# Kernel tuning notes

Hardware: AMD Instinct MI355X
Metric: run time of the kernel (lower is better)

The kernel has to match this reference:

```python
import jax, jax.numpy as jnp
import numpy as np

N, E, R, D_IN, D_H, D_OUT = 75000, 1200000, 8, 64, 64, 40


def setup_inputs() -> dict:
    key = jax.random.key(0)
    k_x, k_idx, k_rel, k_w1, k_w2 = jax.random.split(key, 5)
    x = jax.random.normal(k_x, (N, D_IN), dtype=jnp.float32)
    # Regular-degree CSR pointer: ptr[i+1]-ptr[i] = E//N = 16 (nondecreasing, ptr[0]=0, ptr[N]=E)
    ptr = jnp.arange(N + 1, dtype=jnp.int32) * (E // N)
    idx = jax.random.randint(k_idx, (E,), 0, N, dtype=jnp.int32)   # source node per edge
    rel = jax.random.randint(k_rel, (E,), 0, R, dtype=jnp.int32)   # relation type per edge
    W1 = jax.random.normal(k_w1, (R, D_IN, D_H), dtype=jnp.float32) / np.float32(np.sqrt(D_IN))
    W2 = jax.random.normal(k_w2, (R, D_H, D_OUT), dtype=jnp.float32) / np.float32(np.sqrt(D_H))
    return {"x": x, "ptr": ptr, "idx": idx, "rel": rel, "W1": W1, "W2": W2}


def _rgcn_conv(x, W, idx, rel, dst, num_node):
    # Typed transform for every (node, relation) pair: [N, R, F_out]
    xw = jnp.einsum('nd,rdf->nrf', x, W)
    # Per-edge gather of the relation-specific transformed source feature: [E, F_out]
    msg = xw[idx, rel]
    # Scatter-add into destination nodes (CSR rows)
    return jax.ops.segment_sum(msg, dst, num_segments=num_node)


def reference(x, ptr, idx, rel, W1, W2):
    num_edges = idx.shape[0]
    num_node = ptr.shape[0] - 1
    # CSR row id for each edge e: dst[e] = i s.t. ptr[i] <= e < ptr[i+1]
    dst = jnp.searchsorted(ptr, jnp.arange(num_edges, dtype=ptr.dtype), side='right') - 1
    h = _rgcn_conv(x, W1, idx, rel, dst, num_node)
    h = jax.nn.relu(h)  # dropout is identity in eval mode
    h = _rgcn_conv(h, W2, idx, rel, dst, num_node)
    return jax.nn.log_softmax(h, axis=-1)
```

## Files before the change

### kernel.cpp

```cpp
#include <hip/hip_runtime.h>
#include <hip/hip_bf16.h>


typedef __attribute__((ext_vector_type(8))) short short8;
typedef __attribute__((ext_vector_type(4))) float floatx4;

static __device__ __forceinline__ unsigned short f2bf(float f) {
    unsigned u = __float_as_uint(f);
    u += 0x7FFFu + ((u >> 16) & 1u);
    return (unsigned short)(u >> 16);
}
static __device__ __forceinline__ float bflo(unsigned u) { return __uint_as_float(u << 16); }
static __device__ __forceinline__ float bfhi(unsigned u) { return __uint_as_float(u & 0xffff0000u); }

static __device__ __forceinline__ int sgm(int d) {
    return ((d & 12) << 2) | ((d & 48) >> 2) | (d & 3);
}

__global__ void k_packw(const float* __restrict__ W1, const float* __restrict__ W2,
                        unsigned short* __restrict__ BTf1, unsigned short* __restrict__ BTf2) {
    int i = blockIdx.x * 256 + threadIdx.x;
    if (i < 32768) {
        int chunk = i >> 9, w = i & 511;
        int cb = chunk >> 3, k0 = (chunk >> 2) & 1, g = chunk & 3;
        int lg = w >> 7, lr = (w >> 3) & 15, s = w & 7;
        int j = cb * 64 + g * 16 + lr;
        int d = k0 * 32 + lg * 8 + s;
        int r = j >> 6, f = j & 63;
        BTf1[i] = f2bf(W1[r * 4096 + d * 64 + f]);
    } else if (i < 32768 + 20480) {
        int ii = i - 32768;
        int chunk = ii >> 9, w = ii & 511;
        int cb = chunk >> 3, k0 = (chunk >> 2) & 1, g = chunk & 3;
        int lg = w >> 7, lr = (w >> 3) & 15, s = w & 7;
        int j = cb * 64 + g * 16 + lr;
        int d = k0 * 32 + lg * 8 + s;
        int r = j / 40, f = j - r * 40;
        BTf2[ii] = f2bf(W2[r * 2560 + sgm(d) * 40 + f]);
    }
}

template <int AF32, int NSLAB>
__global__ __launch_bounds__(256) void k_xw(
    const void* __restrict__ Av, const unsigned short* __restrict__ BTf,
    unsigned short* __restrict__ xw, int M) {
    constexpr int NC = NSLAB * 64;
    __shared__ short Bs[NSLAB * 4096];

#pragma unroll
    for (int off = 0; off < NSLAB * 4096; off += 2048)
        *(short8*)(Bs + off + threadIdx.x * 8) =
            *(const short8*)((const short*)BTf + off + threadIdx.x * 8);

    int wave = threadIdx.x >> 6, lane = threadIdx.x & 63;
    int lr = lane & 15, lg = lane >> 4;
    int rowbase = (blockIdx.x * 4 + wave) * 16;
    int row = rowbase + lr;

    short8 af[2];
#pragma unroll
    for (int k0 = 0; k0 < 2; ++k0) {
        int koff = k0 * 32 + lg * 8;
        if constexpr (AF32) {
            const float* Af = (const float*)Av;
            float4 v0 = {0, 0, 0, 0}, v1 = {0, 0, 0, 0};
            if (row < M) {
                v0 = *(const float4*)(Af + (size_t)row * 64 + koff);
                v1 = *(const float4*)(Af + (size_t)row * 64 + koff + 4);
            }
            short8 t;
            t[0] = (short)f2bf(v0.x); t[1] = (short)f2bf(v0.y);
            t[2] = (short)f2bf(v0.z); t[3] = (short)f2bf(v0.w);
            t[4] = (short)f2bf(v1.x); t[5] = (short)f2bf(v1.y);
            t[6] = (short)f2bf(v1.z); t[7] = (short)f2bf(v1.w);
            af[k0] = t;
        } else {
            const unsigned short* Ab = (const unsigned short*)Av;
            af[k0] = *(const short8*)(Ab + (size_t)row * 64 + koff);
        }
    }

    __syncthreads();

#pragma unroll
    for (int cb = 0; cb < NSLAB; ++cb) {
        int col0 = cb * 64;
        floatx4 acc[4] = {};
#pragma unroll
        for (int k0 = 0; k0 < 2; ++k0) {
#pragma unroll
            for (int g = 0; g < 4; ++g) {
                short8 b = *(const short8*)(Bs + ((cb * 2 + k0) * 4 + g) * 512 + lane * 8);
                acc[g] = __builtin_amdgcn_mfma_f32_16x16x32_bf16(b, af[k0], acc[g], 0, 0, 0);
            }
        }
        if constexpr (AF32) {
            short8 o0, o1;
#pragma unroll
            for (int g = 0; g < 2; ++g)
#pragma unroll
                for (int i = 0; i < 4; ++i) {
                    o0[g * 4 + i] = (short)f2bf(acc[g][i]);
                    o1[g * 4 + i] = (short)f2bf(acc[g + 2][i]);
                }
            unsigned short* p = xw + (size_t)row * NC + col0 + lg * 16;
            *(short8*)p = o0;
            *(short8*)(p + 8) = o1;
        } else {
#pragma unroll
            for (int g = 0; g < 4; ++g) {
                unsigned lo = ((unsigned)f2bf(acc[g][1]) << 16) | f2bf(acc[g][0]);
                unsigned hi = ((unsigned)f2bf(acc[g][3]) << 16) | f2bf(acc[g][2]);
                uint2 o = {lo, hi};
                *(uint2*)(xw + (size_t)row * NC + col0 + g * 16 + lg * 4) = o;
            }
        }
    }
}

__global__ __launch_bounds__(256) void k_gs_relu(
    const unsigned short* __restrict__ xw,
    const int* __restrict__ ptr, const int* __restrict__ idx,
    const int* __restrict__ rel,
    unsigned short* __restrict__ H, int M, int MP) {
    int rowA = (blockIdx.x * 4 + (threadIdx.x >> 6)) * 2;
    if (rowA >= MP) return;
    rowA = __builtin_amdgcn_readfirstlane(rowA);
    int lane = threadIdx.x & 63;
    int fl = lane & 31, eo = lane >> 5;
    int rowB = rowA + 1;
    int myrow = eo ? rowB : rowA;
    if (rowA >= M) {
        *(unsigned*)(H + (size_t)myrow * 64 + fl * 2) = 0;
        return;
    }
    float cx = 0.f, cy = 0.f;
    bool both = (rowB < M);
    int p0 = ptr[rowA], p1 = ptr[rowA + 1];
    int p2 = both ? ptr[rowA + 2] : p1;
    if (both && (p1 - p0 == 16) && (p2 - p1 == 16)) {
        const int* ia = idx + p0; const int* ra_ = rel + p0;
        const int* ib = idx + p1; const int* rb_ = rel + p1;
        unsigned u[16];
#pragma unroll
        for (int t = 0; t < 16; ++t) {
            unsigned bA = ((unsigned)ia[t] * 8u + (unsigned)ra_[t]) * 128u;
            unsigned bB = ((unsigned)ib[t] * 8u + (unsigned)rb_[t]) * 128u;
            unsigned b = eo ? bB : bA;
            u[t] = *(const unsigned*)((const char*)xw + b + fl * 4);
        }
#pragma unroll
        for (int t = 0; t < 16; ++t) { cx += bflo(u[t]); cy += bfhi(u[t]); }
    } else {
        int ps = 0, deg = 0;
        if (myrow < M) { ps = ptr[myrow]; deg = ptr[myrow + 1] - ps; }
        for (int t = 0; t < deg; ++t) {
            unsigned b = ((unsigned)idx[ps + t] * 8u + (unsigned)rel[ps + t]) * 128u;
            unsigned u = *(const unsigned*)((const char*)xw + b + fl * 4);
            cx += bflo(u); cy += bfhi(u);
        }
    }
    unsigned o = ((unsigned)f2bf(fmaxf(cy, 0.f)) << 16) | f2bf(fmaxf(cx, 0.f));
    *(unsigned*)(H + (size_t)myrow * 64 + fl * 2) = o;
}

__global__ __launch_bounds__(256) void k_gs_lsm(
    const unsigned short* __restrict__ xw,
    const int* __restrict__ ptr, const int* __restrict__ idx,
    const int* __restrict__ rel,
    float* __restrict__ out, int M) {
    int rowA = (blockIdx.x * 4 + (threadIdx.x >> 6)) * 2;
    if (rowA >= M) return;
    rowA = __builtin_amdgcn_readfirstlane(rowA);
    int lane = threadIdx.x & 63;
    int fl = lane & 31, eo = lane >> 5;
    int rowB = rowA + 1;
    int myrow = eo ? rowB : rowA;
    bool okf = fl < 20;
    int flc = okf ? fl : 0;
    float cx = 0.f, cy = 0.f;
    bool both = (rowB < M);
    int p0 = ptr[rowA], p1 = ptr[rowA + 1];
    int p2 = both ? ptr[rowA + 2] : p1;
    if (both && (p1 - p0 == 16) && (p2 - p1 == 16)) {
        const int* ia = idx + p0; const int* ra_ = rel + p0;
        const int* ib = idx + p1; const int* rb_ = rel + p1;
        unsigned u[16];
#pragma unroll
        for (int t = 0; t < 16; ++t) {
            unsigned bA = ((unsigned)ia[t] * 8u + (unsigned)ra_[t]) * 80u;
            unsigned bB = ((unsigned)ib[t] * 8u + (unsigned)rb_[t]) * 80u;
            unsigned b = eo ? bB : bA;
            u[t] = *(const unsigned*)((const char*)xw + b + flc * 4);
        }
#pragma unroll
        for (int t = 0; t < 16; ++t) { cx += bflo(u[t]); cy += bfhi(u[t]); }
    } else {
        int ps = 0, deg = 0;
        if (myrow < M) { ps = ptr[myrow]; deg = ptr[myrow + 1] - ps; }
        for (int t = 0; t < deg; ++t) {
            unsigned b = ((unsigned)idx[ps + t] * 8u + (unsigned)rel[ps + t]) * 80u;
            unsigned u = *(const unsigned*)((const char*)xw + b + flc * 4);
            cx += bflo(u); cy += bfhi(u);
        }
    }
    float mx = okf ? fmaxf(cx, cy) : -INFINITY;
#pragma unroll
    for (int m = 1; m < 32; m <<= 1) mx = fmaxf(mx, __shfl_xor(mx, m, 32));
    float s = okf ? (__expf(cx - mx) + __expf(cy - mx)) : 0.f;
#pragma unroll
    for (int m = 1; m < 32; m <<= 1) s += __shfl_xor(s, m, 32);
    float lse = mx + __logf(s);
    if (okf && myrow < M) {
        float2 o = {cx - lse, cy - lse};
        *(float2*)(out + (size_t)myrow * 40 + flc * 2) = o;
    }
}

extern "C" void kernel_launch(void* const* d_in, const int* in_sizes, int n_in,
                              void* d_out, int out_size, void* d_ws, size_t ws_size,
                              hipStream_t stream) {
    const float* x  = (const float*)d_in[0];
    const int* ptr  = (const int*)d_in[1];
    const int* idx  = (const int*)d_in[2];
    const int* rel  = (const int*)d_in[3];
    const float* W1 = (const float*)d_in[4];
    const float* W2 = (const float*)d_in[5];
    float* out = (float*)d_out;

    int N = in_sizes[1] - 1;
    int MP = (N + 255) & ~255;

    char* ws = (char*)d_ws;
    size_t szRow64 = (size_t)MP * 64 * 2;
    unsigned short* hbf  = (unsigned short*)ws;
    unsigned short* BTf1 = (unsigned short*)(ws + szRow64);
    unsigned short* BTf2 = BTf1 + 32768;
    unsigned short* xwb  = BTf2 + 20480;

    k_packw<<<(32768 + 20480 + 255) / 256, 256, 0, stream>>>(W1, W2, BTf1, BTf2);

    int nblk = MP / 64;
    k_xw<1, 8><<<nblk, 256, 0, stream>>>((const void*)x, BTf1, xwb, N);
    k_gs_relu<<<MP / 8, 256, 0, stream>>>(xwb, ptr, idx, rel, hbf, N, MP);
    k_xw<0, 5><<<nblk, 256, 0, stream>>>((const void*)hbf, BTf2, xwb, MP);
    k_gs_lsm<<<(N + 7) / 8, 256, 0, stream>>>(xwb, ptr, idx, rel, out, N);
}
```

Baseline: 110.8 us.

## Fuse layer-1 gather/ReLU with layer-2 transform via shared-memory H tile

```diff
diff --git a/kernel.cpp b/kernel.cpp
--- a/kernel.cpp
+++ b/kernel.cpp
@@ -40,15 +40,12 @@
     }
 }
 
-template <int AF32, int NSLAB>
-__global__ __launch_bounds__(256) void k_xw(
-    const void* __restrict__ Av, const unsigned short* __restrict__ BTf,
+__global__ __launch_bounds__(256) void k_xw1(
+    const float* __restrict__ Af, const unsigned short* __restrict__ BTf,
     unsigned short* __restrict__ xw, int M) {
-    constexpr int NC = NSLAB * 64;
-    __shared__ short Bs[NSLAB * 4096];
-
-#pragma unroll
-    for (int off = 0; off < NSLAB * 4096; off += 2048)
+    __shared__ short Bs[8 * 4096];
+#pragma unroll
+    for (int off = 0; off < 8 * 4096; off += 2048)
         *(short8*)(Bs + off + threadIdx.x * 8) =
             *(const short8*)((const short*)BTf + off + threadIdx.x * 8);
 
@@ -61,107 +58,130 @@
 #pragma unroll
     for (int k0 = 0; k0 < 2; ++k0) {
         int koff = k0 * 32 + lg * 8;
-        if constexpr (AF32) {
-            const float* Af = (const float*)Av;
-            float4 v0 = {0, 0, 0, 0}, v1 = {0, 0, 0, 0};
-            if (row < M) {
-                v0 = *(const float4*)(Af + (size_t)row * 64 + koff);
-                v1 = *(const float4*)(Af + (size_t)row * 64 + koff + 4);
-            }
-            short8 t;
-            t[0] = (short)f2bf(v0.x); t[1] = (short)f2bf(v0.y);
-            t[2] = (short)f2bf(v0.z); t[3] = (short)f2bf(v0.w);
-            t[4] = (short)f2bf(v1.x); t[5] = (short)f2bf(v1.y);
-            t[6] = (short)f2bf(v1.z); t[7] = (short)f2bf(v1.w);
-            af[k0] = t;
-        } else {
-            const unsigned short* Ab = (const unsigned short*)Av;
-            af[k0] = *(const short8*)(Ab + (size_t)row * 64 + koff);
-        }
+        float4 v0 = {0, 0, 0, 0}, v1 = {0, 0, 0, 0};
+        if (row < M) {
+            v0 = *(const float4*)(Af + (size_t)row * 64 + koff);
+            v1 = *(const float4*)(Af + (size_t)row * 64 + koff + 4);
+        }
+        short8 t;
+        t[0] = (short)f2bf(v0.x); t[1] = (short)f2bf(v0.y);
+        t[2] = (short)f2bf(v0.z); t[3] = (short)f2bf(v0.w);
+        t[4] = (short)f2bf(v1.x); t[5] = (short)f2bf(v1.y);
+        t[6] = (short)f2bf(v1.z); t[7] = (short)f2bf(v1.w);
+        af[k0] = t;
     }
 
     __syncthreads();
 
 #pragma unroll
-    for (int cb = 0; cb < NSLAB; ++cb) {
+    for (int cb = 0; cb < 8; ++cb) {
         int col0 = cb * 64;
         floatx4 acc[4] = {};
 #pragma unroll
-        for (int k0 = 0; k0 < 2; ++k0) {
+        for (int k0 = 0; k0 < 2; ++k0)
 #pragma unroll
             for (int g = 0; g < 4; ++g) {
                 short8 b = *(const short8*)(Bs + ((cb * 2 + k0) * 4 + g) * 512 + lane * 8);
                 acc[g] = __builtin_amdgcn_mfma_f32_16x16x32_bf16(b, af[k0], acc[g], 0, 0, 0);
             }
-        }
-        if constexpr (AF32) {
-            short8 o0, o1;
-#pragma unroll
-            for (int g = 0; g < 2; ++g)
-#pragma unroll
-                for (int i = 0; i < 4; ++i) {
-                    o0[g * 4 + i] = (short)f2bf(acc[g][i]);
-                    o1[g * 4 + i] = (short)f2bf(acc[g + 2][i]);
-                }
-            unsigned short* p = xw + (size_t)row * NC + col0 + lg * 16;
-            *(short8*)p = o0;
-            *(short8*)(p + 8) = o1;
-        } else {
-#pragma unroll
-            for (int g = 0; g < 4; ++g) {
-                unsigned lo = ((unsigned)f2bf(acc[g][1]) << 16) | f2bf(acc[g][0]);
-                unsigned hi = ((unsigned)f2bf(acc[g][3]) << 16) | f2bf(acc[g][2]);
-                uint2 o = {lo, hi};
-                *(uint2*)(xw + (size_t)row * NC + col0 + g * 16 + lg * 4) = o;
-            }
-        }
-    }
-}
-
-__global__ __launch_bounds__(256) void k_gs_relu(
-    const unsigned short* __restrict__ xw,
+        short8 o0, o1;
+#pragma unroll
+        for (int g = 0; g < 2; ++g)
+#pragma unroll
+            for (int i = 0; i < 4; ++i) {
+                o0[g * 4 + i] = (short)f2bf(acc[g][i]);
+                o1[g * 4 + i] = (short)f2bf(acc[g + 2][i]);
+            }
+        unsigned short* p = xw + (size_t)row * 512 + col0 + lg * 16;
+        *(short8*)p = o0;
+        *(short8*)(p + 8) = o1;
+    }
+}
+
+__global__ __launch_bounds__(512) void k_l2(
+    const unsigned short* __restrict__ xw1,
     const int* __restrict__ ptr, const int* __restrict__ idx,
     const int* __restrict__ rel,
-    unsigned short* __restrict__ H, int M, int MP) {
-    int rowA = (blockIdx.x * 4 + (threadIdx.x >> 6)) * 2;
-    if (rowA >= MP) return;
-    rowA = __builtin_amdgcn_readfirstlane(rowA);
-    int lane = threadIdx.x & 63;
+    const unsigned short* __restrict__ BTf,
+    unsigned short* __restrict__ xw2, int M) {
+    __shared__ short Bs[5 * 4096];
+    __shared__ char Hs[128 * 128];
+
+    int tid = threadIdx.x;
+#pragma unroll
+    for (int i = 0; i < 5; ++i)
+        *(short8*)(Bs + i * 4096 + tid * 8) = *(const short8*)((const short*)BTf + i * 4096 + tid * 8);
+
+    int wid = tid >> 6, lane = tid & 63;
     int fl = lane & 31, eo = lane >> 5;
-    int rowB = rowA + 1;
-    int myrow = eo ? rowB : rowA;
-    if (rowA >= M) {
-        *(unsigned*)(H + (size_t)myrow * 64 + fl * 2) = 0;
-        return;
-    }
-    float cx = 0.f, cy = 0.f;
-    bool both = (rowB < M);
-    int p0 = ptr[rowA], p1 = ptr[rowA + 1];
-    int p2 = both ? ptr[rowA + 2] : p1;
-    if (both && (p1 - p0 == 16) && (p2 - p1 == 16)) {
-        const int* ia = idx + p0; const int* ra_ = rel + p0;
-        const int* ib = idx + p1; const int* rb_ = rel + p1;
-        unsigned u[16];
-#pragma unroll
-        for (int t = 0; t < 16; ++t) {
-            unsigned bA = ((unsigned)ia[t] * 8u + (unsigned)ra_[t]) * 128u;
-            unsigned bB = ((unsigned)ib[t] * 8u + (unsigned)rb_[t]) * 128u;
-            unsigned b = eo ? bB : bA;
-            u[t] = *(const unsigned*)((const char*)xw + b + fl * 4);
-        }
-#pragma unroll
-        for (int t = 0; t < 16; ++t) { cx += bflo(u[t]); cy += bfhi(u[t]); }
-    } else {
-        int ps = 0, deg = 0;
-        if (myrow < M) { ps = ptr[myrow]; deg = ptr[myrow + 1] - ps; }
-        for (int t = 0; t < deg; ++t) {
-            unsigned b = ((unsigned)idx[ps + t] * 8u + (unsigned)rel[ps + t]) * 128u;
-            unsigned u = *(const unsigned*)((const char*)xw + b + fl * 4);
-            cx += bflo(u); cy += bfhi(u);
-        }
-    }
-    unsigned o = ((unsigned)f2bf(fmaxf(cy, 0.f)) << 16) | f2bf(fmaxf(cx, 0.f));
-    *(unsigned*)(H + (size_t)myrow * 64 + fl * 2) = o;
+    int base = blockIdx.x * 128 + wid * 16;
+
+#pragma unroll 2
+    for (int p = 0; p < 8; ++p) {
+        int rowA = base + p * 2, rowB = rowA + 1;
+        int lrow = wid * 16 + p * 2 + eo;
+        float cx = 0.f, cy = 0.f;
+        if (rowA < M) {
+            bool both = (rowB < M);
+            int p0 = ptr[rowA], p1 = ptr[rowA + 1];
+            int p2 = both ? ptr[rowA + 2] : p1;
+            if (both && (p1 - p0 == 16) && (p2 - p1 == 16)) {
+                const int* ia = idx + p0; const int* ra_ = rel + p0;
+                const int* ib = idx + p1; const int* rb_ = rel + p1;
+                unsigned u[16];
+#pragma unroll
+                for (int t = 0; t < 16; ++t) {
+                    unsigned bA = ((unsigned)ia[t] * 8u + (unsigned)ra_[t]) * 128u;
+                    unsigned bB = ((unsigned)ib[t] * 8u + (unsigned)rb_[t]) * 128u;
+                    unsigned b = eo ? bB : bA;
+                    u[t] = *(const unsigned*)((const char*)xw1 + b + fl * 4);
+                }
+#pragma unroll
+                for (int t = 0; t < 16; ++t) { cx += bflo(u[t]); cy += bfhi(u[t]); }
+            } else {
+                int myrow = eo ? rowB : rowA;
+                int ps = 0, deg = 0;
+                if (myrow < M) { ps = ptr[myrow]; deg = ptr[myrow + 1] - ps; }
+                for (int t = 0; t < deg; ++t) {
+                    unsigned b = ((unsigned)idx[ps + t] * 8u + (unsigned)rel[ps + t]) * 128u;
+                    unsigned u = *(const unsigned*)((const char*)xw1 + b + fl * 4);
+                    cx += bflo(u); cy += bfhi(u);
+                }
+            }
+        }
+        unsigned o = ((unsigned)f2bf(fmaxf(cy, 0.f)) << 16) | f2bf(fmaxf(cx, 0.f));
+        *(unsigned*)(Hs + lrow * 128 + ((fl * 4) ^ ((lrow & 7) << 4))) = o;
+    }
+
+    __syncthreads();
+
+    int lr = lane & 15, lg = lane >> 4;
+    int row = base + lr;
+    short8 af[2];
+#pragma unroll
+    for (int k0 = 0; k0 < 2; ++k0)
+        af[k0] = *(const short8*)(Hs + (wid * 16 + lr) * 128 +
+                                  (((k0 * 64 + lg * 16)) ^ ((lr & 7) << 4)));
+
+#pragma unroll
+    for (int cb = 0; cb < 5; ++cb) {
+        int col0 = cb * 64;
+        floatx4 acc[4] = {};
+#pragma unroll
+        for (int k0 = 0; k0 < 2; ++k0)
+#pragma unroll
+            for (int g = 0; g < 4; ++g) {
+                short8 b = *(const short8*)(Bs + ((cb * 2 + k0) * 4 + g) * 512 + lane * 8);
+                acc[g] = __builtin_amdgcn_mfma_f32_16x16x32_bf16(b, af[k0], acc[g], 0, 0, 0);
+            }
+#pragma unroll
+        for (int g = 0; g < 4; ++g) {
+            unsigned lo = ((unsigned)f2bf(acc[g][1]) << 16) | f2bf(acc[g][0]);
+            unsigned hi = ((unsigned)f2bf(acc[g][3]) << 16) | f2bf(acc[g][2]);
+            uint2 o = {lo, hi};
+            *(uint2*)(xw2 + (size_t)row * 320 + col0 + g * 16 + lg * 4) = o;
+        }
+    }
 }
 
 __global__ __launch_bounds__(256) void k_gs_lsm(
@@ -232,17 +252,14 @@
     int MP = (N + 255) & ~255;
 
     char* ws = (char*)d_ws;
-    size_t szRow64 = (size_t)MP * 64 * 2;
-    unsigned short* hbf  = (unsigned short*)ws;
-    unsigned short* BTf1 = (unsigned short*)(ws + szRow64);
+    unsigned short* BTf1 = (unsigned short*)ws;
     unsigned short* BTf2 = BTf1 + 32768;
-    unsigned short* xwb  = BTf2 + 20480;
+    unsigned short* xw1b = BTf2 + 20480;
+    unsigned short* xw2b = xw1b + (size_t)MP * 512;
 
     k_packw<<<(32768 + 20480 + 255) / 256, 256, 0, stream>>>(W1, W2, BTf1, BTf2);
 
-    int nblk = MP / 64;
-    k_xw<1, 8><<<nblk, 256, 0, stream>>>((const void*)x, BTf1, xwb, N);
-    k_gs_relu<<<MP / 8, 256, 0, stream>>>(xwb, ptr, idx, rel, hbf, N, MP);
-    k_xw<0, 5><<<nblk, 256, 0, stream>>>((const void*)hbf, BTf2, xwb, MP);
-    k_gs_lsm<<<(N + 7) / 8, 256, 0, stream>>>(xwb, ptr, idx, rel, out, N);
-}
+    k_xw1<<<MP / 64, 256, 0, stream>>>(x, BTf1, xw1b, N);
+    k_l2<<<MP / 128, 512, 0, stream>>>(xw1b, ptr, idx, rel, BTf2, xw2b, N);
+    k_gs_lsm<<<(N + 7) / 8, 256, 0, stream>>>(xw2b, ptr, idx, rel, out, N);
+}
```

After: 118.8 us. 7.3% more time.
